# Optimization experiments

Measured on AMD Instinct MI355X. Metric: run time of the kernel, lower is better.

## Reference

```python
import jax, jax.numpy as jnp
import numpy as np

H, W = 32, 32
B, C = 32, 256
L = H * W


def _relative_position_index(h, w):
    # Faithful port of the torch buffer construction (meshgrid 'ij').
    ch, cw = np.arange(h), np.arange(w)
    coords = np.stack(np.meshgrid(ch, cw, indexing='ij'))        # [2, h, w]
    cf = coords.reshape(2, -1)                                   # [2, h*w]
    rel = cf[:, :, None] - cf[:, None, :]                        # [2, L, L]
    rel = rel.transpose(1, 2, 0).copy()                          # [L, L, 2]
    rel[:, :, 0] += h - 1
    rel[:, :, 1] += w - 1
    rel[:, :, 0] *= 2 * w - 1
    return rel.sum(-1).astype(np.int32)                          # [L, L]


def setup_inputs() -> dict:
    key = jax.random.key(0)
    kq, kk, kv, ks, kb = jax.random.split(key, 5)
    q = jax.random.normal(kq, (B, C, L), dtype=jnp.float32)
    k = jax.random.normal(kk, (B, C, L), dtype=jnp.float32)
    v = jax.random.normal(kv, (B, C, L), dtype=jnp.float32)
    std = jax.random.normal(ks, (B, C, L), dtype=jnp.float32)
    # Parameter is initialized to zeros in torch; use small randn so bias matters.
    bias_table = jax.random.normal(kb, ((2 * H - 1) * (2 * W - 1),), dtype=jnp.float32) * 0.02
    rel_index = jnp.asarray(_relative_position_index(H, W))
    return {"q": q, "k": k, "v": v, "std": std,
            "bias_table": bias_table, "rel_index": rel_index}


def reference(q, k, v, std, bias_table, rel_index):
    Bq, Cq, Lq = q.shape
    bias = bias_table[rel_index.reshape(-1)].reshape(Lq, Lq)     # [L, L] gather
    scores = jnp.einsum('bci,bcj->bij', q, k) + bias[None]       # [B, L, L]
    S = jax.nn.softmax(scores, axis=-1)
    V = jnp.einsum('bij,bcj->bci', S, v)                         # [B, C, L]
    SD = jnp.einsum('bij,bcj->bci', S, std)                      # [B, C, L]
    return V[:, :, :, None], SD[:, :, :, None]
```

## Files before the change

kernel.cpp:

```cpp
#include <hip/hip_runtime.h>

typedef _Float16 half8 __attribute__((ext_vector_type(8)));
typedef _Float16 half4 __attribute__((ext_vector_type(4)));
typedef float    floatx16 __attribute__((ext_vector_type(16)));

#define MFMA(a, b, c) __builtin_amdgcn_mfma_f32_32x32x16_f16((a), (b), (c), 0, 0, 0)

constexpr int NB = 32, NC = 256, NL = 1024, MI = 32, BJ = 32;
constexpr int NIT = NL / BJ;
constexpr int PSP = 33;

constexpr int OFF_K    = 0;
constexpr int OFF_V    = 16384;
constexpr int OFF_S    = 32768;
constexpr int OFF_PS   = 49152;
constexpr int OFF_PB   = 57600;
constexpr int OFF_ROWS = 59648;
constexpr int SMEM_B   = 60032;

__device__ __forceinline__ int swz(int g) { return g ^ (((g >> 5) & 3) << 1); }

__device__ __forceinline__ void stage_k(_Float16* kF, const float* kb, int tid) {
    #pragma unroll
    for (int r = 0; r < 4; ++r) {
        const int g = tid + r * 256, ks = g >> 6, ls = g & 63;
        const float* src = kb + (size_t)(ks * 16 + (ls >> 5) * 8) * NL + (ls & 31);
        half8 h;
        #pragma unroll
        for (int t = 0; t < 8; ++t) h[t] = (_Float16)src[(size_t)t * NL];
        *(half8*)(kF + g * 8) = h;
    }
}

__device__ __forceinline__ void stage_a(_Float16* dst, const float* base, int tid) {
    #pragma unroll
    for (int r = 0; r < 4; ++r) {
        const int c = (tid >> 2) + r * 64, jc = tid & 3;
        const float* src = base + (size_t)c * NL + jc * 8;
        float4 a = *(const float4*)src;
        float4 b = *(const float4*)(src + 4);
        half8 h;
        h[0] = (_Float16)a.x; h[1] = (_Float16)a.y; h[2] = (_Float16)a.z; h[3] = (_Float16)a.w;
        h[4] = (_Float16)b.x; h[5] = (_Float16)b.y; h[6] = (_Float16)b.z; h[7] = (_Float16)b.w;
        const int gr = ((c >> 5) * 2 + (jc >> 1)) * 64 + (jc & 1) * 32 + (c & 31);
        *(half8*)(dst + swz(gr) * 8) = h;
    }
}

__global__ __launch_bounds__(256, 2)
void att_mfma5(const float* __restrict__ q,
               const float* __restrict__ kk,
               const float* __restrict__ v,
               const float* __restrict__ sd,
               const float* __restrict__ bt,
               const int* __restrict__ ri,
               float* __restrict__ out)
{
    (void)ri;
    __shared__ __align__(16) char smem[SMEM_B];
    _Float16* kF   = (_Float16*)(smem + OFF_K);
    _Float16* vF   = (_Float16*)(smem + OFF_V);
    _Float16* sF   = (_Float16*)(smem + OFF_S);
    float*    pS   = (float*)(smem + OFF_PS);
    _Float16* pB   = (_Float16*)(smem + OFF_PB);
    float*    mrow = (float*)(smem + OFF_ROWS);
    float*    lrow = mrow + 32;
    float*    arow = mrow + 64;

    const int tid  = threadIdx.x;
    const int lane = tid & 63;
    const int wv   = tid >> 6;

    const int bid = blockIdx.x;
    const int b   = (bid & 7) + ((bid >> 8) << 3);
    const int ib  = (bid >> 3) & 31;
    const int i0  = ib * MI;

    const float* kbase = kk + (size_t)b * NC * NL;
    const float* vbase = v  + (size_t)b * NC * NL;
    const float* sbase = sd + (size_t)b * NC * NL;

    half8 qhi[8], qlo[8];
    if (wv < 2) {
        const float* qb = q + (size_t)b * NC * NL + i0 + (lane & 31);
        #pragma unroll
        for (int kk2 = 0; kk2 < 8; ++kk2) {
            const int c0 = (wv * 8 + kk2) * 16 + (lane >> 5) * 8;
            #pragma unroll
            for (int t = 0; t < 8; ++t) {
                float x = qb[(size_t)(c0 + t) * NL];
                _Float16 h = (_Float16)x;
                qhi[kk2][t] = h;
                qlo[kk2][t] = (_Float16)(x - (float)h);
            }
        }
    }
    if (tid < 32) { mrow[tid] = -1e30f; lrow[tid] = 0.0f; arow[tid] = 1.0f; }

    int gA[2][2];
    #pragma unroll
    for (int d = 0; d < 2; ++d) {
        const int ct = wv * 2 + d;
        gA[d][0] = swz(ct * 128 + lane) * 8;
        gA[d][1] = swz(ct * 128 + 64 + lane) * 8;
    }

    floatx16 aV[2], aS[2];
    #pragma unroll
    for (int d = 0; d < 2; ++d)
        #pragma unroll
        for (int r = 0; r < 16; ++r) { aV[d][r] = 0.f; aS[d][r] = 0.f; }

    auto pv_step = [&]() {
        const float al = arow[lane & 31];
        if (!__all(al == 1.0f)) {
            #pragma unroll
            for (int d = 0; d < 2; ++d)
                #pragma unroll
                for (int r = 0; r < 16; ++r) { aV[d][r] *= al; aS[d][r] *= al; }
        }
        half8 pb0 = *(const half8*)(pB + lane * 8);
        half8 pb1 = *(const half8*)(pB + (64 + lane) * 8);
        #pragma unroll
        for (int d = 0; d < 2; ++d) {
            half8 a0 = *(const half8*)(vF + gA[d][0]);
            half8 a1 = *(const half8*)(vF + gA[d][1]);
            aV[d] = MFMA(a0, pb0, aV[d]);
            aV[d] = MFMA(a1, pb1, aV[d]);
            half8 b0 = *(const half8*)(sF + gA[d][0]);
            half8 b1 = *(const half8*)(sF + gA[d][1]);
            aS[d] = MFMA(b0, pb0, aS[d]);
            aS[d] = MFMA(b1, pb1, aS[d]);
        }
    };

    stage_k(kF, kbase, tid);
    __syncthreads();

    for (int it = 0; it < NIT; ++it) {
        const int j0 = it * BJ;

        if (it > 0) pv_step();

        if (wv < 2) {
            floatx16 S;
            #pragma unroll
            for (int r = 0; r < 16; ++r) S[r] = 0.f;
            #pragma unroll
            for (int kk2 = 0; kk2 < 8; ++kk2) {
                const int ks = wv * 8 + kk2;
                half8 bf = *(const half8*)(kF + (ks * 64 + lane) * 8);
                S = MFMA(qhi[kk2], bf, S);
                S = MFMA(qlo[kk2], bf, S);
            }
            float* ps = pS + wv * 32 * PSP + (lane & 31);
            #pragma unroll
            for (int r = 0; r < 16; ++r) {
                int row = (r & 3) + 8 * (r >> 2) + 4 * (lane >> 5);
                ps[row * PSP] = S[r];
            }
        }
        __syncthreads();

        if (it + 1 < NIT) stage_k(kF, kbase + j0 + BJ, tid);
        stage_a(vF, vbase + j0, tid);
        stage_a(sF, sbase + j0, tid);

        {
            const int i = tid >> 3, s = tid & 7;
            const float* ps0 = pS + i * PSP + s * 4;
            const float* bp = bt + (ib - it + 31) * 63 + (i - 4 * s + 28);
            float sc[4];
            sc[0] = ps0[0] + ps0[32 * PSP + 0] + bp[3];
            sc[1] = ps0[1] + ps0[32 * PSP + 1] + bp[2];
            sc[2] = ps0[2] + ps0[32 * PSP + 2] + bp[1];
            sc[3] = ps0[3] + ps0[32 * PSP + 3] + bp[0];
            float lm = fmaxf(fmaxf(sc[0], sc[1]), fmaxf(sc[2], sc[3]));
            lm = fmaxf(lm, __shfl_xor(lm, 1));
            lm = fmaxf(lm, __shfl_xor(lm, 2));
            lm = fmaxf(lm, __shfl_xor(lm, 4));
            const float mo = mrow[i];
            const float mn = fmaxf(lm, mo);
            float sum = 0.f;
            half4 ph;
            #pragma unroll
            for (int x = 0; x < 4; ++x) {
                float e = __expf(sc[x] - mn);
                sum += e;
                ph[x] = (_Float16)e;
            }
            sum += __shfl_xor(sum, 1);
            sum += __shfl_xor(sum, 2);
            sum += __shfl_xor(sum, 4);
            *(half4*)(pB + (((s >> 2) * 64) + ((s >> 1) & 1) * 32 + i) * 8 + (s & 1) * 4) = ph;
            if (s == 0) {
                float al = __expf(mo - mn);
                arow[i] = al;
                lrow[i] = lrow[i] * al + sum;
                mrow[i] = mn;
            }
        }
        __syncthreads();
    }

    pv_step();

    const float linv = 1.0f / lrow[lane & 31];
    float* scr = (float*)smem;
    __syncthreads();
    #pragma unroll
    for (int d = 0; d < 2; ++d) {
        const int ct = wv * 2 + d;
        #pragma unroll
        for (int r = 0; r < 16; ++r) {
            int c = ct * 32 + (r & 3) + 8 * (r >> 2) + 4 * (lane >> 5);
            scr[c * 33 + (lane & 31)] = aV[d][r] * linv;
        }
    }
    __syncthreads();
    {
        float* og = out + ((size_t)b * NC + tid) * NL + i0;
        #pragma unroll
        for (int g = 0; g < 8; ++g) {
            float4 o;
            o.x = scr[tid * 33 + g * 4 + 0];
            o.y = scr[tid * 33 + g * 4 + 1];
            o.z = scr[tid * 33 + g * 4 + 2];
            o.w = scr[tid * 33 + g * 4 + 3];
            *(float4*)(og + g * 4) = o;
        }
    }
    __syncthreads();
    #pragma unroll
    for (int d = 0; d < 2; ++d) {
        const int ct = wv * 2 + d;
        #pragma unroll
        for (int r = 0; r < 16; ++r) {
            int c = ct * 32 + (r & 3) + 8 * (r >> 2) + 4 * (lane >> 5);
            scr[c * 33 + (lane & 31)] = aS[d][r] * linv;
        }
    }
    __syncthreads();
    {
        float* og = out + (size_t)NB * NC * NL + ((size_t)b * NC + tid) * NL + i0;
        #pragma unroll
        for (int g = 0; g < 8; ++g) {
            float4 o;
            o.x = scr[tid * 33 + g * 4 + 0];
            o.y = scr[tid * 33 + g * 4 + 1];
            o.z = scr[tid * 33 + g * 4 + 2];
            o.w = scr[tid * 33 + g * 4 + 3];
            *(float4*)(og + g * 4) = o;
        }
    }
}

extern "C" void kernel_launch(void* const* d_in, const int* in_sizes, int n_in,
                              void* d_out, int out_size, void* d_ws, size_t ws_size,
                              hipStream_t stream)
{
    (void)in_sizes; (void)n_in; (void)d_ws; (void)ws_size; (void)out_size;
    const float* q  = (const float*)d_in[0];
    const float* k  = (const float*)d_in[1];
    const float* v  = (const float*)d_in[2];
    const float* s  = (const float*)d_in[3];
    const float* bt = (const float*)d_in[4];
    const int*   ri = (const int*)d_in[5];
    att_mfma5<<<dim3(NB * (NL / MI)), dim3(256), 0, stream>>>(
        q, k, v, s, bt, ri, (float*)d_out);
}
```

Measured before the change: 399.1 us.

## Prefetch V/std tiles into registers before PV step and split hi/lo accumulators

The global loads for the V and std tiles are now issued at the top of each iteration into registers, before the PV MFMA step and the QK MFMA. The fp16 conversion and LDS store happen after the barrier, so memory latency overlaps with compute. Per-thread address offsets and swizzle indices are hoisted out of the loop. The hi and lo QK MFMAs now accumulate into separate registers, which breaks the serial dependency chain. The cost is 64 extra live float registers per thread, which risks spills or lower occupancy under launch_bounds(256,2).

Result: slower. 597.3 us (+49.6%).

```diff
diff --git a/kernel.cpp b/kernel.cpp
--- a/kernel.cpp
+++ b/kernel.cpp
@@ -32,23 +32,8 @@
     }
 }
 
-__device__ __forceinline__ void stage_a(_Float16* dst, const float* base, int tid) {
-    #pragma unroll
-    for (int r = 0; r < 4; ++r) {
-        const int c = (tid >> 2) + r * 64, jc = tid & 3;
-        const float* src = base + (size_t)c * NL + jc * 8;
-        float4 a = *(const float4*)src;
-        float4 b = *(const float4*)(src + 4);
-        half8 h;
-        h[0] = (_Float16)a.x; h[1] = (_Float16)a.y; h[2] = (_Float16)a.z; h[3] = (_Float16)a.w;
-        h[4] = (_Float16)b.x; h[5] = (_Float16)b.y; h[6] = (_Float16)b.z; h[7] = (_Float16)b.w;
-        const int gr = ((c >> 5) * 2 + (jc >> 1)) * 64 + (jc & 1) * 32 + (c & 31);
-        *(half8*)(dst + swz(gr) * 8) = h;
-    }
-}
-
 __global__ __launch_bounds__(256, 2)
-void att_mfma5(const float* __restrict__ q,
+void att_mfma6(const float* __restrict__ q,
                const float* __restrict__ kk,
                const float* __restrict__ v,
                const float* __restrict__ sd,
@@ -97,6 +82,14 @@
     }
     if (tid < 32) { mrow[tid] = -1e30f; lrow[tid] = 0.0f; arow[tid] = 1.0f; }
 
+    int co[4], swg[4];
+    #pragma unroll
+    for (int r = 0; r < 4; ++r) {
+        const int c = (tid >> 2) + r * 64, jc = tid & 3;
+        co[r] = c * NL + jc * 8;
+        const int gr = ((c >> 5) * 2 + (jc >> 1)) * 64 + (jc & 1) * 32 + (c & 31);
+        swg[r] = swz(gr) * 8;
+    }
     int gA[2][2];
     #pragma unroll
     for (int d = 0; d < 2; ++d) {
@@ -140,31 +133,59 @@
     for (int it = 0; it < NIT; ++it) {
         const int j0 = it * BJ;
 
+        float4 vp0[4], vp1[4], sp0[4], sp1[4];
+        #pragma unroll
+        for (int r = 0; r < 4; ++r) {
+            const float* vs = vbase + co[r] + j0;
+            vp0[r] = *(const float4*)(vs);
+            vp1[r] = *(const float4*)(vs + 4);
+            const float* ss = sbase + co[r] + j0;
+            sp0[r] = *(const float4*)(ss);
+            sp1[r] = *(const float4*)(ss + 4);
+        }
+
         if (it > 0) pv_step();
 
         if (wv < 2) {
-            floatx16 S;
-            #pragma unroll
-            for (int r = 0; r < 16; ++r) S[r] = 0.f;
+            floatx16 Sh, Sl;
+            #pragma unroll
+            for (int r = 0; r < 16; ++r) { Sh[r] = 0.f; Sl[r] = 0.f; }
             #pragma unroll
             for (int kk2 = 0; kk2 < 8; ++kk2) {
                 const int ks = wv * 8 + kk2;
                 half8 bf = *(const half8*)(kF + (ks * 64 + lane) * 8);
-                S = MFMA(qhi[kk2], bf, S);
-                S = MFMA(qlo[kk2], bf, S);
+                Sh = MFMA(qhi[kk2], bf, Sh);
+                Sl = MFMA(qlo[kk2], bf, Sl);
             }
             float* ps = pS + wv * 32 * PSP + (lane & 31);
             #pragma unroll
             for (int r = 0; r < 16; ++r) {
                 int row = (r & 3) + 8 * (r >> 2) + 4 * (lane >> 5);
-                ps[row * PSP] = S[r];
+                ps[row * PSP] = Sh[r] + Sl[r];
             }
         }
         __syncthreads();
 
         if (it + 1 < NIT) stage_k(kF, kbase + j0 + BJ, tid);
-        stage_a(vF, vbase + j0, tid);
-        stage_a(sF, sbase + j0, tid);
+
+        #pragma unroll
+        for (int r = 0; r < 4; ++r) {
+            half8 h;
+            h[0] = (_Float16)vp0[r].x; h[1] = (_Float16)vp0[r].y;
+            h[2] = (_Float16)vp0[r].z; h[3] = (_Float16)vp0[r].w;
+            h[4] = (_Float16)vp1[r].x; h[5] = (_Float16)vp1[r].y;
+            h[6] = (_Float16)vp1[r].z; h[7] = (_Float16)vp1[r].w;
+            *(half8*)(vF + swg[r]) = h;
+        }
+        #pragma unroll
+        for (int r = 0; r < 4; ++r) {
+            half8 h;
+            h[0] = (_Float16)sp0[r].x; h[1] = (_Float16)sp0[r].y;
+            h[2] = (_Float16)sp0[r].z; h[3] = (_Float16)sp0[r].w;
+            h[4] = (_Float16)sp1[r].x; h[5] = (_Float16)sp1[r].y;
+            h[6] = (_Float16)sp1[r].z; h[7] = (_Float16)sp1[r].w;
+            *(half8*)(sF + swg[r]) = h;
+        }
 
         {
             const int i = tid >> 3, s = tid & 7;
@@ -266,6 +287,6 @@
     const float* s  = (const float*)d_in[3];
     const float* bt = (const float*)d_in[4];
     const int*   ri = (const int*)d_in[5];
-    att_mfma5<<<dim3(NB * (NL / MI)), dim3(256), 0, stream>>>(
+    att_mfma6<<<dim3(NB * (NL / MI)), dim3(256), 0, stream>>>(
         q, k, v, s, bt, ri, (float*)d_out);
 }
```
